# Kernel tuning notes

Measured on AMD Instinct MI355X. Metric: run time of the kernel, lower is better.

Reference implementation:

```python
import jax, jax.numpy as jnp
import numpy as np

B, V, K, C = 4, 50000, 128, 128
NNZ = 800000
HID = 256
MLP_C = 3 * C  # x_in | x_diffuse | grad_features


def setup_inputs() -> dict:
    key = jax.random.key(0)
    ks = jax.random.split(key, 24)
    inp = {
        "x_in": jax.random.normal(ks[0], (B, V, C), jnp.float32),
        "evals": jax.random.uniform(ks[1], (B, K), jnp.float32) * 10.0,
        "evecs": jax.random.normal(ks[2], (B, V, K), jnp.float32) / np.sqrt(V),
        "mass": jax.random.uniform(ks[3], (B, V), jnp.float32) + 0.1,
    }
    for i, nm in enumerate(["gradX", "gradY", "gradZ"]):
        inp[nm + "_vals"] = jax.random.normal(ks[4 + 3 * i], (B, NNZ), jnp.float32) * 0.1
        inp[nm + "_rows"] = jax.random.randint(ks[5 + 3 * i], (B, NNZ), 0, V, jnp.int32)
        inp[nm + "_cols"] = jax.random.randint(ks[6 + 3 * i], (B, NNZ), 0, V, jnp.int32)
    # learned parameters
    inp["diffusion_time"] = jax.random.uniform(ks[13], (C,), jnp.float32) * 0.1 + 1e-4
    inp["A_weight"] = jax.random.normal(ks[14], (3 * C, 3 * C), jnp.float32) / np.sqrt(3 * C)
    inp["W0"] = jax.random.normal(ks[15], (HID, MLP_C), jnp.float32) / np.sqrt(MLP_C)
    inp["b0"] = jnp.zeros((HID,), jnp.float32)
    inp["W1"] = jax.random.normal(ks[16], (C, HID), jnp.float32) / np.sqrt(HID)
    inp["b1"] = jnp.zeros((C,), jnp.float32)
    return inp


def _spmm(vals, rows, cols, x):
    # per-mesh sparse (V,V) @ dense (V,C) via gather + segment_sum
    def one(v, r, c, xb):
        return jax.ops.segment_sum(v[:, None] * xb[c], r, num_segments=V)
    return jax.vmap(one)(vals, rows, cols, x)


def reference(x_in, evals, evecs, mass,
              gradX_vals, gradX_rows, gradX_cols,
              gradY_vals, gradY_rows, gradY_cols,
              gradZ_vals, gradZ_rows, gradZ_cols,
              diffusion_time, A_weight, W0, b0, W1, b1):
    # --- LearnedTimeDiffusion ---
    t = jnp.maximum(diffusion_time, 1e-8)                      # clamp
    x_spec = jnp.einsum('bvk,bv,bvc->bkc', evecs, mass, x_in)  # to_basis
    coefs = jnp.exp(-evals[:, :, None] * t[None, None, :])     # (B,K,C)
    x_diffuse = jnp.einsum('bvk,bkc->bvc', evecs, coefs * x_spec)  # from_basis
    # --- spatial gradients (sparse ops) ---
    gx = _spmm(gradX_vals, gradX_rows, gradX_cols, x_diffuse)
    gy = _spmm(gradY_vals, gradY_rows, gradY_cols, x_diffuse)
    gz = _spmm(gradZ_vals, gradZ_rows, gradZ_cols, x_diffuse)
    x_grad = jnp.stack((gx, gy, gz), axis=-1)                  # (B,V,C,3)
    # --- SpatialGradientFeatures ---
    vflat = x_grad.reshape(B, V, 3 * C)
    Av = (vflat @ A_weight.T).reshape(B, V, C, 3)
    grad_feats = jnp.tanh(jnp.sum(x_grad * Av, axis=-1))       # (B,V,C)
    # --- MLP + residual (dropout off / eval mode) ---
    f = jnp.concatenate((x_in, x_diffuse, grad_feats), axis=-1)
    h = jax.nn.relu(f @ W0.T + b0)
    out = h @ W1.T + b1
    return out + x_in
```

## Files before the change

### kernel.cpp

```cpp
#include <hip/hip_runtime.h>
#include <cstdint>
#include <cstddef>

#define B_   4
#define V_   50000
#define VP_  50048
#define VPT_ 50176
#define K_   128
#define C_   128
#define NNZ_ 800000
#define HID_ 256

#define NB_   391
#define CAP_  2560
#define CH_   4096
#define NBF_  196

typedef __attribute__((ext_vector_type(8))) short short8;
typedef __attribute__((ext_vector_type(4))) float f32x4;
typedef unsigned short us;

__device__ __forceinline__ us f2b(float f) {
    union { float f; unsigned u; } v; v.f = f;
    unsigned r = v.u + 0x7fffu + ((v.u >> 16) & 1u);
    return (us)(r >> 16);
}
__device__ __forceinline__ float b2f(us h) {
    union { unsigned u; float f; } v; v.u = ((unsigned)h) << 16; return v.f;
}
__device__ __forceinline__ unsigned pk(float lo, float hi) {
    return (unsigned)f2b(lo) | ((unsigned)f2b(hi) << 16);
}
__device__ __forceinline__ short8 cvt8(float4 p0, float4 p1) {
    union { unsigned u[4]; short8 s; } r;
    r.u[0] = pk(p0.x, p0.y); r.u[1] = pk(p0.z, p0.w);
    r.u[2] = pk(p1.x, p1.y); r.u[3] = pk(p1.z, p1.w);
    return r.s;
}

__global__ __launch_bounds__(256) void k_cvt_all(
    const float* __restrict__ W0, const float* __restrict__ W1,
    const float* __restrict__ Aw,
    us* __restrict__ W0b, us* __restrict__ W1b, us* __restrict__ Awb)
{
    int t = blockIdx.x * 256 + threadIdx.x;
    if (t < 16384) {
        const float* src; us* dst; int i8;
        if (t < 12288) { i8 = t * 8;            src = W0 + i8; dst = W0b + i8; }
        else           { i8 = (t - 12288) * 8;  src = W1 + i8; dst = W1b + i8; }
        float4 x0 = *(const float4*)src;
        float4 x1 = *(const float4*)(src + 4);
        uint4 u;
        u.x = pk(x0.x, x0.y); u.y = pk(x0.z, x0.w);
        u.z = pk(x1.x, x1.y); u.w = pk(x1.z, x1.w);
        *(uint4*)dst = u;
    } else {
        int p  = t - 16384;
        int p1 = p / 384, p2 = p - p1 * 384;
        int q1 = 3 * (p1 & 127) + (p1 >> 7);
        int q2 = 3 * (p2 & 127) + (p2 >> 7);
        Awb[p] = f2b(Aw[q1 * 384 + q2]);
    }
}

__global__ __launch_bounds__(256) void k_trans(
    const float* __restrict__ x_in, const float* __restrict__ mass,
    const float* __restrict__ evecs,
    us* __restrict__ mxT, us* __restrict__ evT, us* __restrict__ fb, int b)
{
    const int v0  = blockIdx.x * 64;
    const int tid = threadIdx.x;
    __shared__ us ts[128][72];

#pragma unroll
    for (int it = 0; it < 8; ++it) {
        int f   = tid + it * 256;
        int row = f >> 5;
        int col = (f & 31) * 4;
        int v   = v0 + row;
        float4 x = make_float4(0.f, 0.f, 0.f, 0.f);
        float  m = 0.f;
        if (v < V_) {
            x = *(const float4*)&x_in[((size_t)b * V_ + v) * C_ + col];
            m = mass[b * V_ + v];
            uint2 u; u.x = pk(x.x, x.y); u.y = pk(x.z, x.w);
            *(uint2*)&fb[(size_t)v * 384 + col] = u;
        }
        ts[col + 0][row] = f2b(x.x * m); ts[col + 1][row] = f2b(x.y * m);
        ts[col + 2][row] = f2b(x.z * m); ts[col + 3][row] = f2b(x.w * m);
    }
    __syncthreads();
    {
        int c = tid >> 1, half = tid & 1;
#pragma unroll
        for (int q = 0; q < 4; ++q) {
            uint4 u = *(const uint4*)&ts[c][half * 32 + q * 8];
            *(uint4*)&mxT[(size_t)c * VPT_ + v0 + half * 32 + q * 8] = u;
        }
    }
    __syncthreads();

#pragma unroll
    for (int it = 0; it < 8; ++it) {
        int f   = tid + it * 256;
        int row = f >> 5;
        int col = (f & 31) * 4;
        int v   = v0 + row;
        float4 e = (v < V_)
            ? *(const float4*)&evecs[((size_t)b * V_ + v) * K_ + col]
            : make_float4(0.f, 0.f, 0.f, 0.f);
        ts[col + 0][row] = f2b(e.x); ts[col + 1][row] = f2b(e.y);
        ts[col + 2][row] = f2b(e.z); ts[col + 3][row] = f2b(e.w);
    }
    __syncthreads();
    {
        int k = tid >> 1, half = tid & 1;
#pragma unroll
        for (int q = 0; q < 4; ++q) {
            uint4 u = *(const uint4*)&ts[k][half * 32 + q * 8];
            *(uint4*)&evT[(size_t)k * VPT_ + v0 + half * 32 + q * 8] = u;
        }
    }
}

__global__ __launch_bounds__(256) void k_spec_mfma(
    const us* __restrict__ evT, const us* __restrict__ mxT,
    float* __restrict__ x_spec, int b)
{
    const int vb  = blockIdx.x * 256;
    const int tid = threadIdx.x;
    const int w   = tid >> 6;
    const int lr  = tid & 15;
    const int lk  = (tid & 63) >> 4;

    f32x4 z = {0.f, 0.f, 0.f, 0.f};
    f32x4 acc[2][8];
#pragma unroll
    for (int mi = 0; mi < 2; ++mi)
#pragma unroll
        for (int ni = 0; ni < 8; ++ni) acc[mi][ni] = z;

#pragma unroll 2
    for (int s = 0; s < 8; ++s) {
        int vo = vb + s * 32 + lk * 8;
        short8 a[2], bf[8];
#pragma unroll
        for (int mi = 0; mi < 2; ++mi)
            a[mi] = *(const short8*)&evT[(size_t)(w * 32 + mi * 16 + lr) * VPT_ + vo];
#pragma unroll
        for (int ni = 0; ni < 8; ++ni)
            bf[ni] = *(const short8*)&mxT[(size_t)(ni * 16 + lr) * VPT_ + vo];
#pragma unroll
        for (int mi = 0; mi < 2; ++mi)
#pragma unroll
            for (int ni = 0; ni < 8; ++ni)
                acc[mi][ni] = __builtin_amdgcn_mfma_f32_16x16x32_bf16(
                    a[mi], bf[ni], acc[mi][ni], 0, 0, 0);
    }
#pragma unroll
    for (int mi = 0; mi < 2; ++mi)
#pragma unroll
        for (int ni = 0; ni < 8; ++ni)
#pragma unroll
            for (int r = 0; r < 4; ++r) {
                int k = w * 32 + mi * 16 + lk * 4 + r;
                int c = ni * 16 + lr;
                atomicAdd(&x_spec[((size_t)b * K_ + k) * C_ + c], acc[mi][ni][r]);
            }
}

__global__ __launch_bounds__(256) void k_scale2(
    const float* __restrict__ evals, const float* __restrict__ dt,
    const float* __restrict__ x_spec, us* __restrict__ spec_t, int b)
{
    int i = blockIdx.x * 256 + threadIdx.x;
    int c = i >> 7;
    int k = i & 127;
    float t = fmaxf(dt[c], 1e-8f);
    float v = __expf(-evals[b * K_ + k] * t) * x_spec[((size_t)b * K_ + k) * C_ + c];
    spec_t[i] = f2b(v);
}

__global__ __launch_bounds__(256) void k_frombasis_mfma(
    const float* __restrict__ evecs, const us* __restrict__ spec_t,
    us* __restrict__ fb, int b)
{
    const int v0  = blockIdx.x * 64;
    const int tid = threadIdx.x;
    const int w   = tid >> 6;
    const int lr  = tid & 15;
    const int lk  = (tid & 63) >> 4;

    f32x4 z = {0.f, 0.f, 0.f, 0.f};
    f32x4 acc[4][2];
#pragma unroll
    for (int mi = 0; mi < 4; ++mi)
#pragma unroll
        for (int ni = 0; ni < 2; ++ni) acc[mi][ni] = z;

#pragma unroll
    for (int ks = 0; ks < 4; ++ks) {
        int ko = ks * 32 + lk * 8;
        short8 a[4], bf[2];
#pragma unroll
        for (int mi = 0; mi < 4; ++mi) {
            int v = v0 + mi * 16 + lr;
            float4 p0 = make_float4(0.f, 0.f, 0.f, 0.f);
            float4 p1 = make_float4(0.f, 0.f, 0.f, 0.f);
            if (v < V_) {
                const float* src = &evecs[((size_t)b * V_ + v) * K_ + ko];
                p0 = *(const float4*)src;
                p1 = *(const float4*)(src + 4);
            }
            a[mi] = cvt8(p0, p1);
        }
#pragma unroll
        for (int ni = 0; ni < 2; ++ni)
            bf[ni] = *(const short8*)&spec_t[(size_t)(w * 32 + ni * 16 + lr) * K_ + ko];
#pragma unroll
        for (int mi = 0; mi < 4; ++mi)
#pragma unroll
            for (int ni = 0; ni < 2; ++ni)
                acc[mi][ni] = __builtin_amdgcn_mfma_f32_16x16x32_bf16(
                    a[mi], bf[ni], acc[mi][ni], 0, 0, 0);
    }
#pragma unroll
    for (int mi = 0; mi < 4; ++mi)
#pragma unroll
        for (int ni = 0; ni < 2; ++ni)
#pragma unroll
            for (int r = 0; r < 4; ++r) {
                int v = v0 + mi * 16 + lk * 4 + r;
                int c = w * 32 + ni * 16 + lr;
                if (v < V_) fb[(size_t)v * 384 + 128 + c] = f2b(acc[mi][ni][r]);
            }
}

__global__ __launch_bounds__(256) void k_binfill(
    const int* __restrict__ r0, const int* __restrict__ r1, const int* __restrict__ r2,
    const int* __restrict__ c0, const int* __restrict__ c1, const int* __restrict__ c2,
    const float* __restrict__ v0, const float* __restrict__ v1, const float* __restrict__ v2,
    uint2* __restrict__ chunk, int* __restrict__ gcnt, int b)
{
    const int d   = blockIdx.y;
    const int e0  = blockIdx.x * CH_;
    const int tid = threadIdx.x;
    const int*   rr = (d == 0) ? r0 : (d == 1) ? r1 : r2;
    const int*   cc = (d == 0) ? c0 : (d == 1) ? c1 : c2;
    const float* vv = (d == 0) ? v0 : (d == 1) ? v1 : v2;

    __shared__ int   hist[NB_];
    __shared__ int   cur[NB_];
    __shared__ int   base[NB_];
    __shared__ int   gbase[NB_];
    __shared__ uint2 buf[CH_];

    for (int i = tid; i < NB_; i += 256) { hist[i] = 0; cur[i] = 0; }
    __syncthreads();

    int rloc[16];
#pragma unroll
    for (int j = 0; j < 16; ++j) {
        int e = e0 + j * 256 + tid;
        int r = (e < NNZ_) ? rr[(size_t)b * NNZ_ + e] : -1;
        rloc[j] = r;
        if (r >= 0) atomicAdd(&hist[r >> 7], 1);
    }
    __syncthreads();

    if (tid < 64) {
        int q0 = tid * 7;
        int loc[7];
        int s = 0;
#pragma unroll
        for (int j = 0; j < 7; ++j) {
            int q = q0 + j;
            int h = (q < NB_) ? hist[q] : 0;
            loc[j] = s; s += h;
        }
        int inc = s;
        for (int off = 1; off < 64; off <<= 1) {
            int t = __shfl_up(inc, off, 64);
            if (tid >= off) inc += t;
        }
        int excl = inc - s;
#pragma unroll
        for (int j = 0; j < 7; ++j) {
            int q = q0 + j;
            if (q < NB_) base[q] = excl + loc[j];
        }
    }
    __syncthreads();

#pragma unroll
    for (int j = 0; j < 16; ++j) {
        int r = rloc[j];
        if (r < 0) continue;
        int e = e0 + j * 256 + tid;
        int q = r >> 7;
        int off = atomicAdd(&cur[q], 1);
        int pos = base[q] + off;
        uint2 ent;
        ent.x = __float_as_uint(vv[(size_t)b * NNZ_ + e]);
        ent.y = ((unsigned)q << 23) | ((unsigned)(r & 127) << 16)
              | (unsigned)cc[(size_t)b * NNZ_ + e];
        buf[pos] = ent;
    }
    __syncthreads();

    for (int q = tid; q < NB_; q += 256) {
        int c = cur[q];
        if (c > 0) gbase[q] = atomicAdd(&gcnt[d * NB_ + q], c);
    }
    __syncthreads();

    const int tot = min(CH_, NNZ_ - e0);
#pragma unroll
    for (int j = 0; j < 16; ++j) {
        int i = tid + j * 256;
        if (i >= tot) break;
        uint2 ent = buf[i];
        int q   = ent.y >> 23;
        int dst = gbase[q] + (i - base[q]);
        if (dst < CAP_)
            chunk[(size_t)(d * NB_ + q) * CAP_ + dst] =
                make_uint2(ent.x, ent.y & 0x7fffffu);
    }
}

__global__ __launch_bounds__(256) void k_sortgather(
    const uint2* __restrict__ chunk, const int* __restrict__ gcnt,
    const us* __restrict__ fb, us* __restrict__ vf)
{
    const int q   = blockIdx.x;
    const int d   = blockIdx.y;
    const int tid = threadIdx.x;
    const int cnt = min(gcnt[d * NB_ + q], CAP_);
    const uint2* cb = chunk + (size_t)(d * NB_ + q) * CAP_;

    __shared__ int   hist[129];
    __shared__ int   lcur[128];
    __shared__ uint2 obuf[CAP_];

    for (int i = tid; i < 128; i += 256) { hist[i] = 0; lcur[i] = 0; }
    __syncthreads();

    uint2 ent[10];
    int n = 0;
    for (int i = tid; i < cnt; i += 256) {
        ent[n] = cb[i];
        atomicAdd(&hist[(ent[n].y >> 16) & 127], 1);
        ++n;
    }
    __syncthreads();

    if (tid < 64) {
        int a0 = hist[tid * 2], a1 = hist[tid * 2 + 1];
        int s = a0 + a1;
        int inc = s;
        for (int off = 1; off < 64; off <<= 1) {
            int t = __shfl_up(inc, off, 64);
            if (tid >= off) inc += t;
        }
        int excl = inc - s;
        hist[tid * 2]     = excl;
        hist[tid * 2 + 1] = excl + a0;
        if (tid == 63) hist[128] = inc;
    }
    __syncthreads();

    for (int j = 0; j < n; ++j) {
        int rl  = (ent[j].y >> 16) & 127;
        int dst = hist[rl] + atomicAdd(&lcur[rl], 1);
        obuf[dst] = make_uint2(ent[j].x, ent[j].y & 0xffffu);
    }
    __syncthreads();

    const int w    = tid >> 6;
    const int lane = tid & 63;
    const int lo2  = lane * 2;
    for (int rl = w; rl < 128; rl += 4) {
        int r = q * 128 + rl;
        if (r >= V_) break;
        int beg = hist[rl], end = hist[rl + 1];

        float ax[8], ay[8];
#pragma unroll
        for (int j = 0; j < 8; ++j) { ax[j] = 0.f; ay[j] = 0.f; }

        int i = beg;
        for (; i + 8 <= end; i += 8) {
            uint2 e[8];
#pragma unroll
            for (int j = 0; j < 8; ++j) e[j] = obuf[i + j];
            unsigned u[8];
#pragma unroll
            for (int j = 0; j < 8; ++j)
                u[j] = *(const unsigned*)&fb[(size_t)e[j].y * 384 + 128 + lo2];
#pragma unroll
            for (int j = 0; j < 8; ++j) {
                float v = __uint_as_float(e[j].x);
                ax[j] += v * b2f((us)(u[j] & 0xffffu));
                ay[j] += v * b2f((us)(u[j] >> 16));
            }
        }
        for (; i < end; ++i) {
            uint2 e0 = obuf[i];
            unsigned u0 = *(const unsigned*)&fb[(size_t)e0.y * 384 + 128 + lo2];
            float v = __uint_as_float(e0.x);
            ax[0] += v * b2f((us)(u0 & 0xffffu));
            ay[0] += v * b2f((us)(u0 >> 16));
        }
        float sx = ((ax[0] + ax[1]) + (ax[2] + ax[3])) + ((ax[4] + ax[5]) + (ax[6] + ax[7]));
        float sy = ((ay[0] + ay[1]) + (ay[2] + ay[3])) + ((ay[4] + ay[5]) + (ay[6] + ay[7]));
        *(unsigned*)&vf[(size_t)r * 384 + d * 128 + lo2] = pk(sx, sy);
    }
}

__global__ __launch_bounds__(256) void k_gf_mfma(
    const us* __restrict__ vf, const us* __restrict__ Awb,
    us* __restrict__ fb)
{
    const int v0  = blockIdx.x * 64;
    const int tid = threadIdx.x;
    const int w   = tid >> 6;
    const int lr  = tid & 15;
    const int lk  = (tid & 63) >> 4;

    f32x4 z = {0.f, 0.f, 0.f, 0.f};
    f32x4 acc[4][3][2];
#pragma unroll
    for (int mi = 0; mi < 4; ++mi)
#pragma unroll
        for (int d = 0; d < 3; ++d)
#pragma unroll
            for (int ci = 0; ci < 2; ++ci) acc[mi][d][ci] = z;

    const us* aa = vf  + (size_t)(v0 + lr) * 384 + lk * 8;
    const us* bb = Awb + (size_t)(w * 32 + lr) * 384 + lk * 8;
#pragma unroll 2
    for (int kc = 0; kc < 12; ++kc) {
        short8 a[4];
#pragma unroll
        for (int mi = 0; mi < 4; ++mi)
            a[mi] = *(const short8*)(aa + mi * (16 * 384) + kc * 32);
        short8 bm[3][2];
#pragma unroll
        for (int d = 0; d < 3; ++d)
#pragma unroll
            for (int ci = 0; ci < 2; ++ci)
                bm[d][ci] = *(const short8*)(bb + (size_t)(d * 128 + ci * 16) * 384 + kc * 32);
#pragma unroll
        for (int mi = 0; mi < 4; ++mi)
#pragma unroll
            for (int d = 0; d < 3; ++d)
#pragma unroll
                for (int ci = 0; ci < 2; ++ci)
                    acc[mi][d][ci] = __builtin_amdgcn_mfma_f32_16x16x32_bf16(
                        a[mi], bm[d][ci], acc[mi][d][ci], 0, 0, 0);
    }
#pragma unroll
    for (int mi = 0; mi < 4; ++mi)
#pragma unroll
        for (int r = 0; r < 4; ++r) {
            int m = mi * 16 + lk * 4 + r;
            int v = v0 + m;
            if (v < V_) {
#pragma unroll
                for (int ci = 0; ci < 2; ++ci) {
                    int c = w * 32 + ci * 16 + lr;
                    float s = 0.f;
#pragma unroll
                    for (int d = 0; d < 3; ++d)
                        s += acc[mi][d][ci][r] * b2f(vf[(size_t)v * 384 + d * 128 + c]);
                    fb[(size_t)v * 384 + 256 + c] = f2b(tanhf(s));
                }
            }
        }
}

__global__ __launch_bounds__(256) void k_mlp_mfma(
    const us* __restrict__ fb,
    const us* __restrict__ W0b, const float* __restrict__ b0,
    const us* __restrict__ W1b, const float* __restrict__ b1,
    const float* __restrict__ x_in, float* __restrict__ out, int b)
{
    const int v0  = blockIdx.x * 64;
    const int tid = threadIdx.x;
    const int w   = tid >> 6;
    const int lr  = tid & 15;
    const int lk  = (tid & 63) >> 4;

    __shared__ us Hs[64][264];

    f32x4 z = {0.f, 0.f, 0.f, 0.f};
    f32x4 acc[4][4];
#pragma unroll
    for (int mi = 0; mi < 4; ++mi)
#pragma unroll
        for (int ni = 0; ni < 4; ++ni) acc[mi][ni] = z;

    const us* fa = fb  + (size_t)(v0 + lr) * 384 + lk * 8;
    const us* wb = W0b + (size_t)(w * 64 + lr) * 384 + lk * 8;
#pragma unroll 4
    for (int kc = 0; kc < 12; ++kc) {
        short8 a[4], bbf[4];
#pragma unroll
        for (int mi = 0; mi < 4; ++mi)
            a[mi] = *(const short8*)(fa + mi * (16 * 384) + kc * 32);
#pragma unroll
        for (int ni = 0; ni < 4; ++ni)
            bbf[ni] = *(const short8*)(wb + ni * (16 * 384) + kc * 32);
#pragma unroll
        for (int mi = 0; mi < 4; ++mi)
#pragma unroll
            for (int ni = 0; ni < 4; ++ni)
                acc[mi][ni] = __builtin_amdgcn_mfma_f32_16x16x32_bf16(
                    a[mi], bbf[ni], acc[mi][ni], 0, 0, 0);
    }
#pragma unroll
    for (int ni = 0; ni < 4; ++ni) {
        int n = w * 64 + ni * 16 + lr;
        float bias = b0[n];
#pragma unroll
        for (int mi = 0; mi < 4; ++mi)
#pragma unroll
            for (int r = 0; r < 4; ++r) {
                int m = mi * 16 + lk * 4 + r;
                Hs[m][n] = f2b(fmaxf(acc[mi][ni][r] + bias, 0.f));
            }
    }
    __syncthreads();

    f32x4 acc2[4][2];
#pragma unroll
    for (int mi = 0; mi < 4; ++mi)
#pragma unroll
        for (int ni = 0; ni < 2; ++ni) acc2[mi][ni] = z;

    const us* w1b = W1b + (size_t)(w * 32 + lr) * 256 + lk * 8;
#pragma unroll 4
    for (int kc = 0; kc < 8; ++kc) {
        short8 a2[4], b2[2];
#pragma unroll
        for (int mi = 0; mi < 4; ++mi)
            a2[mi] = *(const short8*)&Hs[mi * 16 + lr][kc * 32 + lk * 8];
#pragma unroll
        for (int ni = 0; ni < 2; ++ni)
            b2[ni] = *(const short8*)(w1b + ni * (16 * 256) + kc * 32);
#pragma unroll
        for (int mi = 0; mi < 4; ++mi)
#pragma unroll
            for (int ni = 0; ni < 2; ++ni)
                acc2[mi][ni] = __builtin_amdgcn_mfma_f32_16x16x32_bf16(
                    a2[mi], b2[ni], acc2[mi][ni], 0, 0, 0);
    }
#pragma unroll
    for (int ni = 0; ni < 2; ++ni) {
        int n = w * 32 + ni * 16 + lr;
        float bias = b1[n];
#pragma unroll
        for (int mi = 0; mi < 4; ++mi)
#pragma unroll
            for (int r = 0; r < 4; ++r) {
                int m = mi * 16 + lk * 4 + r;
                int v = v0 + m;
                if (v < V_) {
                    size_t o = ((size_t)b * V_ + v) * C_ + n;
                    out[o] = acc2[mi][ni][r] + bias + x_in[o];
                }
            }
    }
}

extern "C" void kernel_launch(void* const* d_in, const int* in_sizes, int n_in,
                              void* d_out, int out_size, void* d_ws, size_t ws_size,
                              hipStream_t stream)
{
    const float* x_in  = (const float*)d_in[0];
    const float* evals = (const float*)d_in[1];
    const float* evecs = (const float*)d_in[2];
    const float* mass  = (const float*)d_in[3];
    const float* gv[3] = {(const float*)d_in[4], (const float*)d_in[7], (const float*)d_in[10]};
    const int*   gr[3] = {(const int*)d_in[5],   (const int*)d_in[8],   (const int*)d_in[11]};
    const int*   gc[3] = {(const int*)d_in[6],   (const int*)d_in[9],   (const int*)d_in[12]};
    const float* dt  = (const float*)d_in[13];
    const float* Aw  = (const float*)d_in[14];
    const float* W0  = (const float*)d_in[15];
    const float* b0  = (const float*)d_in[16];
    const float* W1  = (const float*)d_in[17];
    const float* b1  = (const float*)d_in[18];
    float* out = (float*)d_out;

    float* x_spec = (float*)d_ws;
    us* spec_t = (us*)(x_spec + 65536);
    us* W0b    = spec_t + 16384;
    us* W1b    = W0b + 98304;
    us* Awb    = W1b + 32768;
    us* fb     = Awb + 147456;
    us* vf     = fb + (size_t)VP_ * 384;
    us* evT    = vf + (size_t)VP_ * 384;
    us* mxT    = evT + (size_t)128 * VPT_;
    int* gcnt  = (int*)(mxT + (size_t)128 * VPT_);
    uint2* chunk = (uint2*)evT;

    hipMemsetAsync(x_spec, 0, 65536 * sizeof(float), stream);
    k_cvt_all<<<dim3(640), 256, 0, stream>>>(W0, W1, Aw, W0b, W1b, Awb);

    for (int b = 0; b < B_; ++b) {
        hipMemsetAsync(gcnt, 0, 3 * NB_ * sizeof(int), stream);
        k_trans<<<dim3(784), 256, 0, stream>>>(x_in, mass, evecs, mxT, evT, fb, b);
        k_spec_mfma<<<dim3(196), 256, 0, stream>>>(evT, mxT, x_spec, b);
        k_scale2<<<dim3(64), 256, 0, stream>>>(evals, dt, x_spec, spec_t, b);
        k_frombasis_mfma<<<dim3(782), 256, 0, stream>>>(evecs, spec_t, fb, b);
        k_binfill<<<dim3(NBF_, 3), 256, 0, stream>>>(
            gr[0], gr[1], gr[2], gc[0], gc[1], gc[2], gv[0], gv[1], gv[2],
            chunk, gcnt, b);
        k_sortgather<<<dim3(NB_, 3), 256, 0, stream>>>(chunk, gcnt, fb, vf);
        k_gf_mfma<<<dim3(782), 256, 0, stream>>>(vf, Awb, fb);
        k_mlp_mfma<<<dim3(782), 256, 0, stream>>>(fb, W0b, b0, W1b, b1, x_in, out, b);
    }
}
```

Before: 1.415 ms.

## Fuse evecs/x transpose into spectral MFMA kernel via shared memory

Replaces the separate transpose kernel and spectral projection kernel with one kernel that loads x_in, mass and evecs, converts them to bf16 into shared-memory tiles, and runs the MFMA projection directly. This avoids writing and re-reading the transposed bf16 copies in global memory. The MLP residual now reads the bf16 copy of x_in from the feature buffer instead of fp32 x_in, which saves bandwidth but lowers residual precision. Blocks cover fewer vertices, so there are twice as many atomic adds into x_spec.

```diff
diff --git a/kernel.cpp b/kernel.cpp
--- a/kernel.cpp
+++ b/kernel.cpp
@@ -63,76 +63,20 @@
     }
 }
 
-__global__ __launch_bounds__(256) void k_trans(
+__global__ __launch_bounds__(256) void k_specf(
     const float* __restrict__ x_in, const float* __restrict__ mass,
     const float* __restrict__ evecs,
-    us* __restrict__ mxT, us* __restrict__ evT, us* __restrict__ fb, int b)
-{
-    const int v0  = blockIdx.x * 64;
-    const int tid = threadIdx.x;
-    __shared__ us ts[128][72];
-
-#pragma unroll
-    for (int it = 0; it < 8; ++it) {
-        int f   = tid + it * 256;
-        int row = f >> 5;
-        int col = (f & 31) * 4;
-        int v   = v0 + row;
-        float4 x = make_float4(0.f, 0.f, 0.f, 0.f);
-        float  m = 0.f;
-        if (v < V_) {
-            x = *(const float4*)&x_in[((size_t)b * V_ + v) * C_ + col];
-            m = mass[b * V_ + v];
-            uint2 u; u.x = pk(x.x, x.y); u.y = pk(x.z, x.w);
-            *(uint2*)&fb[(size_t)v * 384 + col] = u;
-        }
-        ts[col + 0][row] = f2b(x.x * m); ts[col + 1][row] = f2b(x.y * m);
-        ts[col + 2][row] = f2b(x.z * m); ts[col + 3][row] = f2b(x.w * m);
-    }
-    __syncthreads();
-    {
-        int c = tid >> 1, half = tid & 1;
-#pragma unroll
-        for (int q = 0; q < 4; ++q) {
-            uint4 u = *(const uint4*)&ts[c][half * 32 + q * 8];
-            *(uint4*)&mxT[(size_t)c * VPT_ + v0 + half * 32 + q * 8] = u;
-        }
-    }
-    __syncthreads();
-
-#pragma unroll
-    for (int it = 0; it < 8; ++it) {
-        int f   = tid + it * 256;
-        int row = f >> 5;
-        int col = (f & 31) * 4;
-        int v   = v0 + row;
-        float4 e = (v < V_)
-            ? *(const float4*)&evecs[((size_t)b * V_ + v) * K_ + col]
-            : make_float4(0.f, 0.f, 0.f, 0.f);
-        ts[col + 0][row] = f2b(e.x); ts[col + 1][row] = f2b(e.y);
-        ts[col + 2][row] = f2b(e.z); ts[col + 3][row] = f2b(e.w);
-    }
-    __syncthreads();
-    {
-        int k = tid >> 1, half = tid & 1;
-#pragma unroll
-        for (int q = 0; q < 4; ++q) {
-            uint4 u = *(const uint4*)&ts[k][half * 32 + q * 8];
-            *(uint4*)&evT[(size_t)k * VPT_ + v0 + half * 32 + q * 8] = u;
-        }
-    }
-}
-
-__global__ __launch_bounds__(256) void k_spec_mfma(
-    const us* __restrict__ evT, const us* __restrict__ mxT,
-    float* __restrict__ x_spec, int b)
-{
-    const int vb  = blockIdx.x * 256;
+    float* __restrict__ x_spec, us* __restrict__ fb, int b)
+{
+    const int vb  = blockIdx.x * 128;
     const int tid = threadIdx.x;
     const int w   = tid >> 6;
     const int lr  = tid & 15;
     const int lk  = (tid & 63) >> 4;
 
+    __shared__ us ev_t[128][40];
+    __shared__ us mx_t[128][40];
+
     f32x4 z = {0.f, 0.f, 0.f, 0.f};
     f32x4 acc[2][8];
 #pragma unroll
@@ -140,22 +84,45 @@
 #pragma unroll
         for (int ni = 0; ni < 8; ++ni) acc[mi][ni] = z;
 
-#pragma unroll 2
-    for (int s = 0; s < 8; ++s) {
-        int vo = vb + s * 32 + lk * 8;
-        short8 a[2], bf[8];
+    for (int s = 0; s < 4; ++s) {
+        int v0 = vb + s * 32;
+        __syncthreads();
+#pragma unroll
+        for (int it = 0; it < 4; ++it) {
+            int f   = tid + it * 256;
+            int row = f >> 5;
+            int col = (f & 31) * 4;
+            int v   = v0 + row;
+            float4 x = make_float4(0.f, 0.f, 0.f, 0.f);
+            float4 e = make_float4(0.f, 0.f, 0.f, 0.f);
+            float  m = 0.f;
+            if (v < V_) {
+                x = *(const float4*)&x_in [((size_t)b * V_ + v) * C_ + col];
+                e = *(const float4*)&evecs[((size_t)b * V_ + v) * K_ + col];
+                m = mass[b * V_ + v];
+                uint2 u; u.x = pk(x.x, x.y); u.y = pk(x.z, x.w);
+                *(uint2*)&fb[(size_t)v * 384 + col] = u;
+            }
+            mx_t[col + 0][row] = f2b(x.x * m); mx_t[col + 1][row] = f2b(x.y * m);
+            mx_t[col + 2][row] = f2b(x.z * m); mx_t[col + 3][row] = f2b(x.w * m);
+            ev_t[col + 0][row] = f2b(e.x); ev_t[col + 1][row] = f2b(e.y);
+            ev_t[col + 2][row] = f2b(e.z); ev_t[col + 3][row] = f2b(e.w);
+        }
+        __syncthreads();
+
+        short8 a[2], bf8[8];
 #pragma unroll
         for (int mi = 0; mi < 2; ++mi)
-            a[mi] = *(const short8*)&evT[(size_t)(w * 32 + mi * 16 + lr) * VPT_ + vo];
+            a[mi] = *(const short8*)&ev_t[w * 32 + mi * 16 + lr][lk * 8];
 #pragma unroll
         for (int ni = 0; ni < 8; ++ni)
-            bf[ni] = *(const short8*)&mxT[(size_t)(ni * 16 + lr) * VPT_ + vo];
+            bf8[ni] = *(const short8*)&mx_t[ni * 16 + lr][lk * 8];
 #pragma unroll
         for (int mi = 0; mi < 2; ++mi)
 #pragma unroll
             for (int ni = 0; ni < 8; ++ni)
                 acc[mi][ni] = __builtin_amdgcn_mfma_f32_16x16x32_bf16(
-                    a[mi], bf[ni], acc[mi][ni], 0, 0, 0);
+                    a[mi], bf8[ni], acc[mi][ni], 0, 0, 0);
     }
 #pragma unroll
     for (int mi = 0; mi < 2; ++mi)
@@ -483,7 +450,7 @@
     const us* __restrict__ fb,
     const us* __restrict__ W0b, const float* __restrict__ b0,
     const us* __restrict__ W1b, const float* __restrict__ b1,
-    const float* __restrict__ x_in, float* __restrict__ out, int b)
+    float* __restrict__ out, int b)
 {
     const int v0  = blockIdx.x * 64;
     const int tid = threadIdx.x;
@@ -566,8 +533,8 @@
                 int m = mi * 16 + lk * 4 + r;
                 int v = v0 + m;
                 if (v < V_) {
-                    size_t o = ((size_t)b * V_ + v) * C_ + n;
-                    out[o] = acc2[mi][ni][r] + bias + x_in[o];
+                    float xi = b2f(fb[(size_t)v * 384 + n]);
+                    out[((size_t)b * V_ + v) * C_ + n] = acc2[mi][ni][r] + bias + xi;
                 }
             }
     }
@@ -599,18 +566,16 @@
     us* Awb    = W1b + 32768;
     us* fb     = Awb + 147456;
     us* vf     = fb + (size_t)VP_ * 384;
-    us* evT    = vf + (size_t)VP_ * 384;
-    us* mxT    = evT + (size_t)128 * VPT_;
-    int* gcnt  = (int*)(mxT + (size_t)128 * VPT_);
-    uint2* chunk = (uint2*)evT;
+    us* scratch = vf + (size_t)VP_ * 384;
+    int* gcnt  = (int*)(scratch + (size_t)256 * VPT_);
+    uint2* chunk = (uint2*)scratch;
 
     hipMemsetAsync(x_spec, 0, 65536 * sizeof(float), stream);
     k_cvt_all<<<dim3(640), 256, 0, stream>>>(W0, W1, Aw, W0b, W1b, Awb);
 
     for (int b = 0; b < B_; ++b) {
         hipMemsetAsync(gcnt, 0, 3 * NB_ * sizeof(int), stream);
-        k_trans<<<dim3(784), 256, 0, stream>>>(x_in, mass, evecs, mxT, evT, fb, b);
-        k_spec_mfma<<<dim3(196), 256, 0, stream>>>(evT, mxT, x_spec, b);
+        k_specf<<<dim3(392), 256, 0, stream>>>(x_in, mass, evecs, x_spec, fb, b);
         k_scale2<<<dim3(64), 256, 0, stream>>>(evals, dt, x_spec, spec_t, b);
         k_frombasis_mfma<<<dim3(782), 256, 0, stream>>>(evecs, spec_t, fb, b);
         k_binfill<<<dim3(NBF_, 3), 256, 0, stream>>>(
@@ -618,6 +583,6 @@
             chunk, gcnt, b);
         k_sortgather<<<dim3(NB_, 3), 256, 0, stream>>>(chunk, gcnt, fb, vf);
         k_gf_mfma<<<dim3(782), 256, 0, stream>>>(vf, Awb, fb);
-        k_mlp_mfma<<<dim3(782), 256, 0, stream>>>(fb, W0b, b0, W1b, b1, x_in, out, b);
-    }
-}
+        k_mlp_mfma<<<dim3(782), 256, 0, stream>>>(fb, W0b, b0, W1b, b1, out, b);
+    }
+}
```

New measurement: 1.348 ms. 4.7% less time.
